# Kernel tuning notes

Hardware: AMD Instinct MI355X
Metric: run time of the kernel (lower is better)

Reference implementation:

```python
import jax, jax.numpy as jnp
import numpy as np

B, S, H, T, NF = 64, 512, 1024, 4, 12
P = NF * (NF - 1) // 2  # 66 step pairs


def _head(x, w1, b1, w2, b2):
    # LinearsHead (eval mode: dropout = identity): linear -> relu -> linear
    return jax.nn.relu(x @ w1 + b1) @ w2 + b2


def setup_inputs() -> dict:
    key = jax.random.key(0)
    ks = jax.random.split(key, 12)
    sc = 0.02
    # non-overlapping contiguous spans: targets then facts, each L tokens
    L = S // (T + NF)  # 32
    t_start = jnp.arange(T, dtype=jnp.int32) * L
    f_start = (T + jnp.arange(NF, dtype=jnp.int32)) * L
    target_offsets = jnp.broadcast_to(jnp.stack([t_start, t_start + L], -1), (B, T, 2))
    fact_offsets = jnp.broadcast_to(jnp.stack([f_start, f_start + L], -1), (B, NF, 2))
    return {
        'seq_features': jax.random.normal(ks[0], (B, S, H), jnp.float32),
        'cls_features': jax.random.normal(ks[1], (B, H), jnp.float32),
        'target_offsets': target_offsets,
        'fact_offsets': fact_offsets,
        'fact_score_mask': jnp.ones((B, NF, T), jnp.float32),
        'sentsim_w1': sc * jax.random.normal(ks[2], (2 * H, H), jnp.float32),
        'sentsim_b1': jnp.zeros((H,), jnp.float32),
        'sentsim_w2': sc * jax.random.normal(ks[3], (H, 1), jnp.float32),
        'sentsim_b2': jnp.zeros((1,), jnp.float32),
        'step_w1': sc * jax.random.normal(ks[4], (2 * H, H), jnp.float32),
        'step_b1': jnp.zeros((H,), jnp.float32),
        'step_w2': sc * jax.random.normal(ks[5], (H, 1), jnp.float32),
        'step_b2': jnp.zeros((1,), jnp.float32),
        'state_w1': sc * jax.random.normal(ks[6], (H, H), jnp.float32),
        'state_b1': jnp.zeros((H,), jnp.float32),
        'state_w2': sc * jax.random.normal(ks[7], (H, 1), jnp.float32),
        'state_b2': jnp.zeros((1,), jnp.float32),
        'abd_w1': sc * jax.random.normal(ks[8], (2 * H, H), jnp.float32),
        'abd_b1': jnp.zeros((H,), jnp.float32),
        'abd_w2': sc * jax.random.normal(ks[9], (H, 1), jnp.float32),
        'abd_b2': jnp.zeros((1,), jnp.float32),
        'lambda_weight': jnp.array([0.5, 0.5], jnp.float32),
    }


def reference(seq_features, cls_features, target_offsets, fact_offsets, fact_score_mask,
              sentsim_w1, sentsim_b1, sentsim_w2, sentsim_b2,
              step_w1, step_b1, step_w2, step_b2,
              state_w1, state_b1, state_w2, state_b2,
              abd_w1, abd_b1, abd_w2, abd_b2, lambda_weight):
    b, s, h = seq_features.shape
    t = target_offsets.shape[1]
    nf = fact_offsets.shape[1]
    pos = jnp.arange(s)

    def seg_mean(offs):  # offs [b,k,2] -> mean-pooled [b,k,h]
        m = ((pos >= offs[..., 0:1]) & (pos < offs[..., 1:2])).astype(seq_features.dtype)
        cnt = (offs[..., 1] - offs[..., 0]).astype(seq_features.dtype)[..., None]
        return jnp.einsum('bks,bsh->bkh', m, seq_features) / cnt

    tgt = seg_mean(target_offsets)  # [b,t,h]
    fct = seg_mean(fact_offsets)    # [b,nf,h]

    # fact-cls pairs ordered target-major: features[ti*nf+fi] = cat(fact, target)
    ff = jnp.broadcast_to(fct[:, None], (b, t, nf, h))
    tt = jnp.broadcast_to(tgt[:, :, None], (b, t, nf, h))
    pair = jnp.concatenate([ff, tt], -1).reshape(b, t * nf, 2 * h)
    fact_score = jax.nn.sigmoid(_head(pair, sentsim_w1, sentsim_b1, sentsim_w2, sentsim_b2)[..., 0])  # [b, t*nf]
    # original does .view(len(facts), len(targets)) on the flat t-major scores
    mat = fact_score.reshape(b, nf, t)
    max_per_fact = jnp.max(mat * fact_score_mask, axis=2)  # [b, nf]
    state_fact = jnp.mean(max_per_fact, axis=1)            # [b]
    state_cls = jax.nn.sigmoid(_head(cls_features, state_w1, state_b1, state_w2, state_b2)[..., 0])
    w = jax.nn.softmax(lambda_weight)
    state = w[0] * state_fact + w[1] * state_cls           # [b]

    # step pairs: combinations(range(nf), 2) == row-major triu indices
    i1, i2 = jnp.triu_indices(nf, k=1)
    step_feat = jnp.concatenate([fct[:, i1], fct[:, i2]], -1)  # [b,P,2h]
    step = _head(step_feat, step_w1, step_b1, step_w2, step_b2)[..., 0]  # [b,P]

    tside = jnp.mean(tgt, axis=1)  # sum/len over targets [b,h]
    abd_feat = jnp.concatenate([jnp.broadcast_to(tside[:, None], (b, nf, h)), fct], -1)
    abd = _head(abd_feat, abd_w1, abd_b1, abd_w2, abd_b2)[..., 0]  # [b,nf]

    # step_func == 'softmax_all': joint softmax over step + abd scores
    allsc = jax.nn.softmax(jnp.concatenate([step, abd], axis=1), axis=1)
    np_pairs = i1.shape[0]
    step, abd = allsc[:, :np_pairs], allsc[:, np_pairs:]

    # pack: [state | fact_score | step | step_abd]
    return jnp.concatenate([state[:, None], fact_score, step, abd], axis=1)
```

## Files before the change

kernel.cpp:

```cpp
#include <hip/hip_runtime.h>
#include <hip/hip_bf16.h>

#define B_    64
#define S_    512
#define H_    1024
#define HH_   (H_*H_)
#define T_    4
#define NF_   12
#define TNF_  48
#define NP_   66
#define OUTC_ 127

#define NSENT_ (B_*TNF_)
#define NSTEP_ (B_*NP_)
#define NABD_  (B_*NF_)
#define NCLS_  (B_)
#define NWAVES_ (NSENT_+NSTEP_+NABD_+NCLS_)

#define AROW_FCT   0
#define AROW_TGT   768
#define AROW_TSD   1024
#define AROW_CLS   1088
#define AROWS_PAD_ 1280

#define GROW_FSENT 0
#define GROW_S1    768
#define GROW_S2    1536
#define GROW_AF    2304
#define GROW_TSENT 3072
#define GROW_AT    3328
#define GROW_CLS   3392
#define GROWS_     3456

typedef __bf16 bf16x8 __attribute__((ext_vector_type(8)));
typedef float  f32x4  __attribute__((ext_vector_type(4)));
typedef __attribute__((address_space(1))) const unsigned int gcu32;
typedef __attribute__((address_space(3))) unsigned int lu32;

__device__ __forceinline__ ushort f2bf(float x) {
    union { float f; unsigned u; } c; c.f = x;
    unsigned r = c.u + 0x7fffu + ((c.u >> 16) & 1u);
    return (ushort)(r >> 16);
}
__device__ __forceinline__ float bflo(unsigned u) {
    union { unsigned u; float f; } c; c.u = u << 16; return c.f;
}
__device__ __forceinline__ float bfhi(unsigned u) {
    union { unsigned u; float f; } c; c.u = u & 0xffff0000u; return c.f;
}

__global__ __launch_bounds__(256) void prep_kernel(
    const float* __restrict__ seq, const int* __restrict__ toffs,
    const int* __restrict__ foffs, const float* __restrict__ cls,
    const float* __restrict__ sw1, const float* __restrict__ pw1,
    const float* __restrict__ aw1, const float* __restrict__ cw1,
    float* __restrict__ tgt32, ushort* __restrict__ Abf,
    ushort* __restrict__ Wt)
{
    int blk = blockIdx.x;
    int tid = threadIdx.x;

    if (blk < 1024) {
        int b = blk >> 4;
        int k = blk & 15;
        int start, end, arow;
        float* dst32 = nullptr;
        if (k < T_) {
            start = toffs[(b*T_ + k)*2];
            end   = toffs[(b*T_ + k)*2 + 1];
            dst32 = tgt32 + (size_t)(b*T_ + k) * H_;
            arow  = AROW_TGT + b*T_ + k;
        } else {
            int f = k - T_;
            start = foffs[(b*NF_ + f)*2];
            end   = foffs[(b*NF_ + f)*2 + 1];
            arow  = AROW_FCT + b*NF_ + f;
        }
        int h0 = tid * 4;
        const float* base = seq + ((size_t)b * S_ + start) * H_ + h0;
        float4 s = make_float4(0.f, 0.f, 0.f, 0.f);
        int n = end - start;
        #pragma unroll 4
        for (int r = 0; r < n; ++r) {
            float4 v = *(const float4*)(base + (size_t)r * H_);
            s.x += v.x; s.y += v.y; s.z += v.z; s.w += v.w;
        }
        float inv = 1.f / (float)n;
        s.x *= inv; s.y *= inv; s.z *= inv; s.w *= inv;
        if (dst32) *(float4*)(dst32 + h0) = s;
        ushort4 q; q.x = f2bf(s.x); q.y = f2bf(s.y); q.z = f2bf(s.z); q.w = f2bf(s.w);
        *(ushort4*)(Abf + (size_t)arow * H_ + h0) = q;
    } else if (blk < 1088) {
        int b = blk - 1024;
        int h0 = tid * 4;
        float4 c = *(const float4*)(cls + (size_t)b * H_ + h0);
        ushort4 qc; qc.x = f2bf(c.x); qc.y = f2bf(c.y); qc.z = f2bf(c.z); qc.w = f2bf(c.w);
        *(ushort4*)(Abf + (size_t)(AROW_CLS + b) * H_ + h0) = qc;
    } else {
        __shared__ float Tt[32][33];
        int idx2 = blk - 1088;
        int z = idx2 >> 10;
        int rem = idx2 & 1023;
        int k0 = (rem >> 5) * 32;
        int n0 = (rem & 31) * 32;
        const float* src;
        switch (z) {
            case 0: src = sw1; break;
            case 1: src = pw1; break;
            case 2: src = pw1 + HH_; break;
            case 3: src = aw1 + HH_; break;
            case 4: src = sw1 + HH_; break;
            case 5: src = aw1; break;
            default: src = cw1; break;
        }
        int ty = tid >> 3, tx = tid & 7;
        float4 v = *(const float4*)(src + (size_t)(k0 + ty) * H_ + n0 + tx*4);
        Tt[ty][tx*4 + 0] = v.x; Tt[ty][tx*4 + 1] = v.y;
        Tt[ty][tx*4 + 2] = v.z; Tt[ty][tx*4 + 3] = v.w;
        __syncthreads();
        int nx = ty, kx = tx;
        ushort4 q;
        q.x = f2bf(Tt[kx*4 + 0][nx]); q.y = f2bf(Tt[kx*4 + 1][nx]);
        q.z = f2bf(Tt[kx*4 + 2][nx]); q.w = f2bf(Tt[kx*4 + 3][nx]);
        *(ushort4*)(Wt + (size_t)z * HH_ + (size_t)(n0 + nx) * H_ + k0 + kx*4) = q;
    }
}

__global__ __launch_bounds__(256) void tside_kernel(
    const float* __restrict__ tgt32, ushort* __restrict__ Abf)
{
    int b = blockIdx.x;
    int h0 = threadIdx.x * 4;
    float4 s = make_float4(0.f, 0.f, 0.f, 0.f);
    for (int t = 0; t < T_; ++t) {
        float4 v = *(const float4*)(tgt32 + (size_t)(b*T_ + t)*H_ + h0);
        s.x += v.x; s.y += v.y; s.z += v.z; s.w += v.w;
    }
    ushort4 q;
    q.x = f2bf(s.x*0.25f); q.y = f2bf(s.y*0.25f);
    q.z = f2bf(s.z*0.25f); q.w = f2bf(s.w*0.25f);
    *(ushort4*)(Abf + (size_t)(AROW_TSD + b) * H_ + h0) = q;
}

__global__ __launch_bounds__(256) void gemm_bf16_kernel(
    const ushort* __restrict__ Abf, const ushort* __restrict__ Wt,
    ushort* __restrict__ G)
{
    __shared__ __align__(16) ushort As[2][128*32];
    __shared__ __align__(16) ushort Bs[2][128*32];

    int bx = blockIdx.x;
    int arow_base, wsel, grow_base, m0, vrows;
    if (bx < 24)      { int j = bx / 6; int mt = bx % 6; arow_base = AROW_FCT;
                        wsel = j; grow_base = j * 768; m0 = mt * 128; vrows = 128; }
    else if (bx < 26) { arow_base = AROW_TGT; wsel = 4; grow_base = GROW_TSENT;
                        m0 = (bx - 24) * 128; vrows = 128; }
    else if (bx == 26){ arow_base = AROW_TSD; wsel = 5; grow_base = GROW_AT;
                        m0 = 0; vrows = 64; }
    else              { arow_base = AROW_CLS; wsel = 6; grow_base = GROW_CLS;
                        m0 = 0; vrows = 64; }

    const int tid  = threadIdx.x;
    const int lane = tid & 63;
    const int w    = tid >> 6;
    const int wr   = w >> 1, wc = w & 1;
    const int n0   = blockIdx.y * 128;

    const int srow = lane >> 2;
    const int scol = ((lane & 3) ^ ((lane >> 3) & 3)) * 8;
    const ushort* gA0 = Abf + (size_t)(arow_base + m0 + w*16 + srow) * H_ + scol;
    const ushort* gA1 = gA0 + (size_t)64 * H_;
    const ushort* gB0 = Wt + (size_t)wsel * HH_
                        + (size_t)(n0 + w*16 + srow) * H_ + scol;
    const ushort* gB1 = gB0 + (size_t)64 * H_;
    const int ldsA0 = (0*64 + w*16) * 32, ldsA1 = (1*64 + w*16) * 32;

    const int frr  = lane & 15;
    const int c0   = lane >> 4;
    const int swz  = (frr >> 1) & 3;
    const int offA = (wr*64 + frr) * 32 + (c0 ^ swz) * 8;
    const int offB = (wc*64 + frr) * 32 + (c0 ^ swz) * 8;

    f32x4 acc[4][4];
    #pragma unroll
    for (int i = 0; i < 4; ++i)
        #pragma unroll
        for (int j = 0; j < 4; ++j)
            acc[i][j] = (f32x4){0.f, 0.f, 0.f, 0.f};

    #define STAGE(buf, kstep) do {                                              \
        int kk_ = (kstep) < 32 ? (kstep) * 32 : 0;                              \
        __builtin_amdgcn_global_load_lds((gcu32*)(gA0 + kk_),                   \
            (lu32*)(As[buf] + ldsA0), 16, 0, 0);                                \
        __builtin_amdgcn_global_load_lds((gcu32*)(gA1 + kk_),                   \
            (lu32*)(As[buf] + ldsA1), 16, 0, 0);                                \
        __builtin_amdgcn_global_load_lds((gcu32*)(gB0 + kk_),                   \
            (lu32*)(Bs[buf] + ldsA0), 16, 0, 0);                                \
        __builtin_amdgcn_global_load_lds((gcu32*)(gB1 + kk_),                   \
            (lu32*)(Bs[buf] + ldsA1), 16, 0, 0);                                \
    } while (0)

    STAGE(0, 0);
    STAGE(1, 1);

    #pragma unroll 1
    for (int t = 0; t < 32; ++t) {
        const int cur = t & 1;
        asm volatile("s_waitcnt vmcnt(4)" ::: "memory");
        __builtin_amdgcn_s_barrier();
        __builtin_amdgcn_sched_barrier(0);

        const ushort* pa = As[cur] + offA;
        const ushort* pb = Bs[cur] + offB;
        bf16x8 a0 = *(const bf16x8*)(pa);
        bf16x8 a1 = *(const bf16x8*)(pa + 16*32);
        bf16x8 a2 = *(const bf16x8*)(pa + 32*32);
        bf16x8 a3 = *(const bf16x8*)(pa + 48*32);
        bf16x8 b0 = *(const bf16x8*)(pb);
        bf16x8 b1 = *(const bf16x8*)(pb + 16*32);
        bf16x8 b2 = *(const bf16x8*)(pb + 32*32);
        bf16x8 b3 = *(const bf16x8*)(pb + 48*32);

        asm volatile("s_waitcnt lgkmcnt(0)" ::: "memory");
        __builtin_amdgcn_s_barrier();
        __builtin_amdgcn_sched_barrier(0);

        if (t < 30) STAGE(cur, t + 2);

        bf16x8 av[4] = {a0, a1, a2, a3};
        bf16x8 bv[4] = {b0, b1, b2, b3};
        #pragma unroll
        for (int i = 0; i < 4; ++i)
            #pragma unroll
            for (int j = 0; j < 4; ++j)
                acc[i][j] = __builtin_amdgcn_mfma_f32_16x16x32_bf16(
                    av[i], bv[j], acc[i][j], 0, 0, 0);
    }
    #undef STAGE

    const int r0 = (lane >> 4) * 4;
    const int cc = lane & 15;
    #pragma unroll
    for (int i = 0; i < 4; ++i) {
        int lrow = wr*64 + i*16 + r0;
        if (lrow >= vrows) continue;
        #pragma unroll
        for (int r = 0; r < 4; ++r) {
            size_t gr = (size_t)(grow_base + m0 + lrow + r) * H_ + n0 + wc*64 + cc;
            #pragma unroll
            for (int j = 0; j < 4; ++j)
                G[gr + j*16] = f2bf(acc[i][j][r]);
        }
    }
}

__global__ __launch_bounds__(256) void combine_kernel(
    const ushort* __restrict__ G,
    const float* __restrict__ sb1, const float* __restrict__ sw2,
    const float* __restrict__ pb1, const float* __restrict__ pw2,
    const float* __restrict__ ab1, const float* __restrict__ aw2,
    const float* __restrict__ cb1, const float* __restrict__ cw2,
    float* __restrict__ ssent, float* __restrict__ sstep,
    float* __restrict__ sabd, float* __restrict__ scls)
{
    int wv = blockIdx.x * 4 + (threadIdx.x >> 6);
    int lane = threadIdx.x & 63;
    if (wv >= NWAVES_) return;

    const ushort *U, *V;
    const float *b1, *w2;
    float* outp;
    if (wv < NSENT_) {
        int b = wv / TNF_, q = wv % TNF_;
        int t = q / NF_, f = q % NF_;
        U = G + (size_t)(GROW_FSENT + b*NF_ + f) * H_;
        V = G + (size_t)(GROW_TSENT + b*T_ + t) * H_;
        b1 = sb1; w2 = sw2; outp = ssent + wv;
    } else if (wv < NSENT_ + NSTEP_) {
        int s = wv - NSENT_;
        int b = s / NP_, p = s % NP_;
        int i = 0, rem = p, cnt = NF_ - 1;
        while (rem >= cnt) { rem -= cnt; --cnt; ++i; }
        int j = i + 1 + rem;
        U = G + (size_t)(GROW_S1 + b*NF_ + i) * H_;
        V = G + (size_t)(GROW_S2 + b*NF_ + j) * H_;
        b1 = pb1; w2 = pw2; outp = sstep + s;
    } else if (wv < NSENT_ + NSTEP_ + NABD_) {
        int s = wv - NSENT_ - NSTEP_;
        int b = s / NF_, f = s % NF_;
        U = G + (size_t)(GROW_AT + b) * H_;
        V = G + (size_t)(GROW_AF + b*NF_ + f) * H_;
        b1 = ab1; w2 = aw2; outp = sabd + s;
    } else {
        int b = wv - NSENT_ - NSTEP_ - NABD_;
        U = G + (size_t)(GROW_CLS + b) * H_;
        V = nullptr;
        b1 = cb1; w2 = cw2; outp = scls + b;
    }

    float acc = 0.f;
    #pragma unroll
    for (int h = 0; h < 2; ++h) {
        int nb = h * 512 + lane * 8;
        uint4 uu = *(const uint4*)(U + nb);
        float us[8] = { bflo(uu.x), bfhi(uu.x), bflo(uu.y), bfhi(uu.y),
                        bflo(uu.z), bfhi(uu.z), bflo(uu.w), bfhi(uu.w) };
        if (V) {
            uint4 vv = *(const uint4*)(V + nb);
            us[0] += bflo(vv.x); us[1] += bfhi(vv.x);
            us[2] += bflo(vv.y); us[3] += bfhi(vv.y);
            us[4] += bflo(vv.z); us[5] += bfhi(vv.z);
            us[6] += bflo(vv.w); us[7] += bfhi(vv.w);
        }
        float4 bA = *(const float4*)(b1 + nb);
        float4 bB = *(const float4*)(b1 + nb + 4);
        float4 wA = *(const float4*)(w2 + nb);
        float4 wB = *(const float4*)(w2 + nb + 4);
        acc = fmaf(fmaxf(us[0] + bA.x, 0.f), wA.x, acc);
        acc = fmaf(fmaxf(us[1] + bA.y, 0.f), wA.y, acc);
        acc = fmaf(fmaxf(us[2] + bA.z, 0.f), wA.z, acc);
        acc = fmaf(fmaxf(us[3] + bA.w, 0.f), wA.w, acc);
        acc = fmaf(fmaxf(us[4] + bB.x, 0.f), wB.x, acc);
        acc = fmaf(fmaxf(us[5] + bB.y, 0.f), wB.y, acc);
        acc = fmaf(fmaxf(us[6] + bB.z, 0.f), wB.z, acc);
        acc = fmaf(fmaxf(us[7] + bB.w, 0.f), wB.w, acc);
    }
    #pragma unroll
    for (int msk = 1; msk < 64; msk <<= 1)
        acc += __shfl_xor(acc, msk);
    if (lane == 0) *outp = acc;
}

__global__ __launch_bounds__(128) void finalize_kernel(
    const float* __restrict__ s_sent, const float* __restrict__ s_step,
    const float* __restrict__ s_abd, const float* __restrict__ s_cls,
    const float* __restrict__ mask, const float* __restrict__ lam,
    const float* __restrict__ sent_b2, const float* __restrict__ step_b2,
    const float* __restrict__ state_b2, const float* __restrict__ abd_b2,
    float* __restrict__ out)
{
    int b = blockIdx.x;
    int tid = threadIdx.x;
    __shared__ float fs[TNF_];
    __shared__ float sc[NP_ + NF_];
    __shared__ float mpf[NF_];
    __shared__ float smax, ssum;

    if (tid < TNF_) {
        float v = 1.f / (1.f + expf(-(s_sent[b*TNF_ + tid] + sent_b2[0])));
        fs[tid] = v;
        out[(size_t)b*OUTC_ + 1 + tid] = v;
    }
    if (tid < NP_)
        sc[tid] = s_step[b*NP_ + tid] + step_b2[0];
    else if (tid < NP_ + NF_)
        sc[tid] = s_abd[b*NF_ + (tid - NP_)] + abd_b2[0];
    __syncthreads();

    if (tid < NF_) {
        float m = -1e30f;
        for (int j = 0; j < T_; ++j)
            m = fmaxf(m, fs[tid*T_ + j] * mask[((size_t)b*NF_ + tid)*T_ + j]);
        mpf[tid] = m;
    }
    __syncthreads();

    if (tid == 0) {
        float sf = 0.f;
        for (int i = 0; i < NF_; ++i) sf += mpf[i];
        sf *= (1.f / NF_);
        float scls2 = 1.f / (1.f + expf(-(s_cls[b] + state_b2[0])));
        float l0 = lam[0], l1 = lam[1];
        float mx = fmaxf(l0, l1);
        float e0 = expf(l0 - mx), e1 = expf(l1 - mx);
        float w0 = e0 / (e0 + e1);
        out[(size_t)b*OUTC_] = w0 * sf + (1.f - w0) * scls2;
        float m2 = -1e30f;
        for (int i = 0; i < NP_ + NF_; ++i) m2 = fmaxf(m2, sc[i]);
        smax = m2;
    }
    __syncthreads();
    if (tid < NP_ + NF_) sc[tid] = expf(sc[tid] - smax);
    __syncthreads();
    if (tid == 0) {
        float s2 = 0.f;
        for (int i = 0; i < NP_ + NF_; ++i) s2 += sc[i];
        ssum = s2;
    }
    __syncthreads();
    if (tid < NP_ + NF_)
        out[(size_t)b*OUTC_ + 1 + TNF_ + tid] = sc[tid] / ssum;
}

extern "C" void kernel_launch(void* const* d_in, const int* in_sizes, int n_in,
                              void* d_out, int out_size, void* d_ws, size_t ws_size,
                              hipStream_t stream)
{
    (void)in_sizes; (void)n_in; (void)out_size; (void)ws_size;
    const float* seq  = (const float*)d_in[0];
    const float* cls  = (const float*)d_in[1];
    const int*   toff = (const int*)d_in[2];
    const int*   foff = (const int*)d_in[3];
    const float* mask = (const float*)d_in[4];
    const float* sw1  = (const float*)d_in[5];
    const float* sb1  = (const float*)d_in[6];
    const float* sw2  = (const float*)d_in[7];
    const float* sb2  = (const float*)d_in[8];
    const float* pw1  = (const float*)d_in[9];
    const float* pb1  = (const float*)d_in[10];
    const float* pw2  = (const float*)d_in[11];
    const float* pb2  = (const float*)d_in[12];
    const float* cw1  = (const float*)d_in[13];
    const float* cb1  = (const float*)d_in[14];
    const float* cw2  = (const float*)d_in[15];
    const float* cb2  = (const float*)d_in[16];
    const float* aw1  = (const float*)d_in[17];
    const float* ab1  = (const float*)d_in[18];
    const float* aw2  = (const float*)d_in[19];
    const float* ab2  = (const float*)d_in[20];
    const float* lam  = (const float*)d_in[21];

    char* wsb = (char*)d_ws;
    float*  tgt32 = (float*)wsb;
    float*  ssent = (float*)(wsb + (1u<<20));
    float*  sstep = ssent + NSENT_;
    float*  sabd  = sstep + NSTEP_;
    float*  scls  = sabd + NABD_;
    ushort* Abf   = (ushort*)(wsb + (1u<<20) + 32768);
    ushort* Wt    = Abf + (size_t)AROWS_PAD_ * H_;
    ushort* G     = Wt + (size_t)7 * HH_;

    prep_kernel<<<1088 + 7*1024, 256, 0, stream>>>(
        seq, toff, foff, cls, sw1, pw1, aw1, cw1, tgt32, Abf, Wt);

    tside_kernel<<<B_, 256, 0, stream>>>(tgt32, Abf);

    gemm_bf16_kernel<<<dim3(28, 8), 256, 0, stream>>>(Abf, Wt, G);

    combine_kernel<<<(NWAVES_ + 3) / 4, 256, 0, stream>>>(
        G, sb1, sw2, pb1, pw2, ab1, aw2, cb1, cw2,
        ssent, sstep, sabd, scls);

    finalize_kernel<<<B_, 128, 0, stream>>>(
        ssent, sstep, sabd, scls, mask, lam, sb2, pb2, cb2, ab2, (float*)d_out);
}
```

Baseline: 62.45 us.

## Deepen GEMM LDS pipeline to four stages and linearize block grid

The bf16 GEMM moves from a double-buffered LDS pipeline to a four-buffer ring with three tiles in flight. Each k-step now needs one barrier instead of two, and the prefetch is issued before the MFMA work. The 2D grid is flattened to 224 blocks so the eight N-tiles that share an A tile are launched next to each other, which should improve L2 reuse. LDS use doubles to 64KB per block, which may lower occupancy.

```diff
diff --git a/kernel.cpp b/kernel.cpp
--- a/kernel.cpp
+++ b/kernel.cpp
@@ -146,25 +146,33 @@
     const ushort* __restrict__ Abf, const ushort* __restrict__ Wt,
     ushort* __restrict__ G)
 {
-    __shared__ __align__(16) ushort As[2][128*32];
-    __shared__ __align__(16) ushort Bs[2][128*32];
-
-    int bx = blockIdx.x;
-    int arow_base, wsel, grow_base, m0, vrows;
-    if (bx < 24)      { int j = bx / 6; int mt = bx % 6; arow_base = AROW_FCT;
-                        wsel = j; grow_base = j * 768; m0 = mt * 128; vrows = 128; }
-    else if (bx < 26) { arow_base = AROW_TGT; wsel = 4; grow_base = GROW_TSENT;
-                        m0 = (bx - 24) * 128; vrows = 128; }
-    else if (bx == 26){ arow_base = AROW_TSD; wsel = 5; grow_base = GROW_AT;
-                        m0 = 0; vrows = 64; }
-    else              { arow_base = AROW_CLS; wsel = 6; grow_base = GROW_CLS;
-                        m0 = 0; vrows = 64; }
+    __shared__ __align__(16) ushort As[4][128*32];
+    __shared__ __align__(16) ushort Bs[4][128*32];
+
+    const int id = blockIdx.x;
+    int arow_base, wsel, grow_base, m0, vrows, by;
+    if (id < 192) {
+        int j = id / 48, r = id % 48, mt = r >> 3;
+        by = r & 7;
+        arow_base = AROW_FCT; wsel = j; grow_base = j * 768;
+        m0 = mt * 128; vrows = 128;
+    } else if (id < 208) {
+        int r = id - 192; int mtt = r >> 3; by = r & 7;
+        arow_base = AROW_TGT; wsel = 4; grow_base = GROW_TSENT;
+        m0 = mtt * 128; vrows = 128;
+    } else if (id < 216) {
+        by = id & 7;
+        arow_base = AROW_TSD; wsel = 5; grow_base = GROW_AT; m0 = 0; vrows = 64;
+    } else {
+        by = id & 7;
+        arow_base = AROW_CLS; wsel = 6; grow_base = GROW_CLS; m0 = 0; vrows = 64;
+    }
 
     const int tid  = threadIdx.x;
     const int lane = tid & 63;
     const int w    = tid >> 6;
     const int wr   = w >> 1, wc = w & 1;
-    const int n0   = blockIdx.y * 128;
+    const int n0   = by * 128;
 
     const int srow = lane >> 2;
     const int scol = ((lane & 3) ^ ((lane >> 3) & 3)) * 8;
@@ -189,7 +197,7 @@
             acc[i][j] = (f32x4){0.f, 0.f, 0.f, 0.f};
 
     #define STAGE(buf, kstep) do {                                              \
-        int kk_ = (kstep) < 32 ? (kstep) * 32 : 0;                              \
+        int kk_ = (kstep) * 32;                                                 \
         __builtin_amdgcn_global_load_lds((gcu32*)(gA0 + kk_),                   \
             (lu32*)(As[buf] + ldsA0), 16, 0, 0);                                \
         __builtin_amdgcn_global_load_lds((gcu32*)(gA1 + kk_),                   \
@@ -200,43 +208,52 @@
             (lu32*)(Bs[buf] + ldsA1), 16, 0, 0);                                \
     } while (0)
 
+    #define COMPUTE(cur) do {                                                   \
+        const ushort* pa = As[cur] + offA;                                      \
+        const ushort* pb = Bs[cur] + offB;                                      \
+        bf16x8 a0 = *(const bf16x8*)(pa);                                       \
+        bf16x8 a1 = *(const bf16x8*)(pa + 16*32);                               \
+        bf16x8 a2 = *(const bf16x8*)(pa + 32*32);                               \
+        bf16x8 a3 = *(const bf16x8*)(pa + 48*32);                               \
+        bf16x8 b0 = *(const bf16x8*)(pb);                                       \
+        bf16x8 b1 = *(const bf16x8*)(pb + 16*32);                               \
+        bf16x8 b2 = *(const bf16x8*)(pb + 32*32);                               \
+        bf16x8 b3 = *(const bf16x8*)(pb + 48*32);                               \
+        asm volatile("s_waitcnt lgkmcnt(0)" ::: "memory");                      \
+        __builtin_amdgcn_sched_barrier(0);                                      \
+        bf16x8 av[4] = {a0, a1, a2, a3};                                        \
+        bf16x8 bv[4] = {b0, b1, b2, b3};                                        \
+        _Pragma("unroll")                                                       \
+        for (int i = 0; i < 4; ++i)                                             \
+            _Pragma("unroll")                                                   \
+            for (int j = 0; j < 4; ++j)                                         \
+                acc[i][j] = __builtin_amdgcn_mfma_f32_16x16x32_bf16(            \
+                    av[i], bv[j], acc[i][j], 0, 0, 0);                          \
+    } while (0)
+
     STAGE(0, 0);
     STAGE(1, 1);
+    STAGE(2, 2);
 
     #pragma unroll 1
-    for (int t = 0; t < 32; ++t) {
-        const int cur = t & 1;
-        asm volatile("s_waitcnt vmcnt(4)" ::: "memory");
+    for (int t = 0; t < 30; ++t) {
+        asm volatile("s_waitcnt vmcnt(8)" ::: "memory");
         __builtin_amdgcn_s_barrier();
         __builtin_amdgcn_sched_barrier(0);
-
-        const ushort* pa = As[cur] + offA;
-        const ushort* pb = Bs[cur] + offB;
-        bf16x8 a0 = *(const bf16x8*)(pa);
-        bf16x8 a1 = *(const bf16x8*)(pa + 16*32);
-        bf16x8 a2 = *(const bf16x8*)(pa + 32*32);
-        bf16x8 a3 = *(const bf16x8*)(pa + 48*32);
-        bf16x8 b0 = *(const bf16x8*)(pb);
-        bf16x8 b1 = *(const bf16x8*)(pb + 16*32);
-        bf16x8 b2 = *(const bf16x8*)(pb + 32*32);
-        bf16x8 b3 = *(const bf16x8*)(pb + 48*32);
-
-        asm volatile("s_waitcnt lgkmcnt(0)" ::: "memory");
-        __builtin_amdgcn_s_barrier();
-        __builtin_amdgcn_sched_barrier(0);
-
-        if (t < 30) STAGE(cur, t + 2);
-
-        bf16x8 av[4] = {a0, a1, a2, a3};
-        bf16x8 bv[4] = {b0, b1, b2, b3};
-        #pragma unroll
-        for (int i = 0; i < 4; ++i)
-            #pragma unroll
-            for (int j = 0; j < 4; ++j)
-                acc[i][j] = __builtin_amdgcn_mfma_f32_16x16x32_bf16(
-                    av[i], bv[j], acc[i][j], 0, 0, 0);
-    }
+        if (t < 29) STAGE((t + 3) & 3, t + 3);
+        COMPUTE(t & 3);
+    }
+    asm volatile("s_waitcnt vmcnt(4)" ::: "memory");
+    __builtin_amdgcn_s_barrier();
+    __builtin_amdgcn_sched_barrier(0);
+    COMPUTE(2);
+    asm volatile("s_waitcnt vmcnt(0)" ::: "memory");
+    __builtin_amdgcn_s_barrier();
+    __builtin_amdgcn_sched_barrier(0);
+    COMPUTE(3);
+
     #undef STAGE
+    #undef COMPUTE
 
     const int r0 = (lane >> 4) * 4;
     const int cc = lane & 15;
@@ -435,7 +452,7 @@
 
     tside_kernel<<<B_, 256, 0, stream>>>(tgt32, Abf);
 
-    gemm_bf16_kernel<<<dim3(28, 8), 256, 0, stream>>>(Abf, Wt, G);
+    gemm_bf16_kernel<<<224, 256, 0, stream>>>(Abf, Wt, G);
 
     combine_kernel<<<(NWAVES_ + 3) / 4, 256, 0, stream>>>(
         G, sb1, sw2, pb1, pw2, ab1, aw2, cb1, cw2,
```

After: 64.89 us. 3.9% more time.
